# Optimization experiments

Measured on AMD Instinct MI355X. Metric: run time of the kernel, lower is better.

Reference implementation:

```python
import jax, jax.numpy as jnp
import numpy as np

N_USER = 50_000
N_ITEM = 100_000
N = N_USER + N_ITEM          # total graph nodes
E = 2_400_000                # nnz of normalized adjacency (avg degree ~16)
D = 64                       # emb_size; layers = [64, 64, 64]
SLOPE = 0.2                  # NGCF uses LeakyReLU(alpha=0.2)


def setup_inputs() -> dict:
    key = jax.random.key(0)
    ks = jax.random.split(key, 20)
    inp = {
        "user_emb": jax.random.normal(ks[0], (N_USER, D), jnp.float32) * 0.1,
        "item_emb": jax.random.normal(ks[1], (N_ITEM, D), jnp.float32) * 0.1,
    }
    for k in range(3):
        inp[f"W_gc_{k}"] = jax.random.normal(ks[2 + 4 * k], (D, D), jnp.float32) * 0.1
        inp[f"b_gc_{k}"] = jax.random.normal(ks[3 + 4 * k], (1, D), jnp.float32) * 0.1
        inp[f"W_bi_{k}"] = jax.random.normal(ks[4 + 4 * k], (D, D), jnp.float32) * 0.1
        inp[f"b_bi_{k}"] = jax.random.normal(ks[5 + 4 * k], (1, D), jnp.float32) * 0.1
    inp["adj_vals"] = jax.random.uniform(ks[14], (E,), jnp.float32) * (1.0 / 16.0)
    inp["adj_rows"] = jax.random.randint(ks[15], (E,), 0, N, jnp.int32)
    inp["adj_cols"] = jax.random.randint(ks[16], (E,), 0, N, jnp.int32)
    return inp


def _l2norm(x):
    n = jnp.linalg.norm(x, axis=1, keepdims=True)
    return x / jnp.maximum(n, 1e-12)


def reference(user_emb, item_emb,
              W_gc_0, b_gc_0, W_bi_0, b_bi_0,
              W_gc_1, b_gc_1, W_bi_1, b_bi_1,
              W_gc_2, b_gc_2, W_bi_2, b_bi_2,
              adj_vals, adj_rows, adj_cols):
    Wg = [W_gc_0, W_gc_1, W_gc_2]
    bg = [b_gc_0, b_gc_1, b_gc_2]
    Wb = [W_bi_0, W_bi_1, W_bi_2]
    bb = [b_bi_0, b_bi_1, b_bi_2]

    ego = jnp.concatenate([user_emb, item_emb], axis=0)  # [N, D]
    all_embs = [ego]
    for k in range(3):
        # side = norm_adj @ ego  (sparse COO spmm via gather + segment_sum)
        msgs = adj_vals[:, None] * ego[adj_cols]          # [E, D]
        side = jax.ops.segment_sum(msgs, adj_rows, num_segments=N)
        sum_emb = jax.nn.leaky_relu(side @ Wg[k] + bg[k], SLOPE)
        bi_emb = jax.nn.leaky_relu((ego * side) @ Wb[k] + bb[k], SLOPE)
        ego = sum_emb + bi_emb
        all_embs.append(_l2norm(ego))
    return jnp.concatenate(all_embs, axis=1)              # [N, 4*D]
```

## Files before the change

kernel.cpp:

```cpp
#include <hip/hip_runtime.h>

#define N_TOT      150000
#define N_USER     50000
#define N_EDGE     2400000
#define DIM        64
#define OUT_STRIDE 256
#define SLOPE      0.2f
#define NB_SCAN    ((N_TOT + 255) / 256)


__global__ void init_ego(const float* __restrict__ ue, const float* __restrict__ ie,
                         float* __restrict__ ego, float* __restrict__ out) {
    int idx = blockIdx.x * blockDim.x + threadIdx.x;
    if (idx >= N_TOT * DIM / 4) return;
    int n  = idx >> 4;
    int c4 = idx & 15;
    float4 v = (n < N_USER) ? ((const float4*)ue)[idx]
                            : ((const float4*)ie)[idx - N_USER * (DIM / 4)];
    ((float4*)ego)[idx] = v;
    ((float4*)out)[n * (OUT_STRIDE / 4) + c4] = v;
}

__global__ void hist_rank(const int* __restrict__ rows, int* __restrict__ cnt,
                          int* __restrict__ rank) {
    int t = blockIdx.x * blockDim.x + threadIdx.x;
    if (t >= N_EDGE / 4) return;
    int4 r4 = ((const int4*)rows)[t];
    int4 k4;
    k4.x = atomicAdd(&cnt[r4.x], 1);
    k4.y = atomicAdd(&cnt[r4.y], 1);
    k4.z = atomicAdd(&cnt[r4.z], 1);
    k4.w = atomicAdd(&cnt[r4.w], 1);
    ((int4*)rank)[t] = k4;
}

__global__ __launch_bounds__(256) void scan_partial(const int* __restrict__ cnt,
                                                    int* __restrict__ row_ptr,
                                                    int* __restrict__ bsum) {
    __shared__ int s[256];
    int tid = threadIdx.x;
    int i = blockIdx.x * 256 + tid;
    int v = (i < N_TOT) ? cnt[i] : 0;
    s[tid] = v;
    __syncthreads();
    for (int off = 1; off < 256; off <<= 1) {
        int t = (tid >= off) ? s[tid - off] : 0;
        __syncthreads();
        s[tid] += t;
        __syncthreads();
    }
    if (i < N_TOT) row_ptr[i] = s[tid] - v;
    if (tid == 255) bsum[blockIdx.x] = s[255];
}

__global__ __launch_bounds__(1024) void scan_bsums(int* __restrict__ bsum) {
    __shared__ int s[1024];
    int tid = threadIdx.x;
    int v = (tid < NB_SCAN) ? bsum[tid] : 0;
    s[tid] = v;
    __syncthreads();
    for (int off = 1; off < 1024; off <<= 1) {
        int t = (tid >= off) ? s[tid - off] : 0;
        __syncthreads();
        s[tid] += t;
        __syncthreads();
    }
    if (tid < NB_SCAN) bsum[tid] = s[tid] - v;
}

__global__ __launch_bounds__(256) void add_offsets(int* __restrict__ row_ptr,
                                                   const int* __restrict__ bsum) {
    int i = blockIdx.x * 256 + threadIdx.x;
    if (i < N_TOT) row_ptr[i] += bsum[blockIdx.x];
    if (i == 0) row_ptr[N_TOT] = N_EDGE;
}

__global__ void scatter_edges(const int* __restrict__ rows, const int* __restrict__ cols,
                              const float* __restrict__ vals,
                              const int* __restrict__ row_ptr,
                              const int* __restrict__ rank, int2* __restrict__ epack) {
    int t = blockIdx.x * blockDim.x + threadIdx.x;
    if (t >= N_EDGE / 4) return;
    int4   r4 = ((const int4*)rows)[t];
    int4   k4 = ((const int4*)rank)[t];
    int4   c4 = ((const int4*)cols)[t];
    float4 v4 = ((const float4*)vals)[t];
    epack[row_ptr[r4.x] + k4.x] = make_int2(c4.x, __float_as_int(v4.x));
    epack[row_ptr[r4.y] + k4.y] = make_int2(c4.y, __float_as_int(v4.y));
    epack[row_ptr[r4.z] + k4.z] = make_int2(c4.z, __float_as_int(v4.z));
    epack[row_ptr[r4.w] + k4.w] = make_int2(c4.w, __float_as_int(v4.w));
}

__global__ __launch_bounds__(256) void spmm_gather(
    const int* __restrict__ row_ptr, const int2* __restrict__ epack,
    const float* __restrict__ ego, float* __restrict__ side) {
    int lane = threadIdx.x & 63;
    int row  = blockIdx.x * 4 + (threadIdx.x >> 6);
    if (row >= N_TOT) return;
    int beg = row_ptr[row];
    int end = row_ptr[row + 1];
    int g = lane >> 4;
    int q = lane & 15;
    float4 acc = make_float4(0.f, 0.f, 0.f, 0.f);
    int i = beg;
    for (; i + 16 <= end; i += 16) {
        int4 e0 = ((const int4*)(epack + i))[g];
        int4 e1 = ((const int4*)(epack + i + 8))[g];
        float4 va = ((const float4*)(ego + (size_t)e0.x * DIM))[q];
        float4 vb = ((const float4*)(ego + (size_t)e0.z * DIM))[q];
        float4 vc = ((const float4*)(ego + (size_t)e1.x * DIM))[q];
        float4 vd = ((const float4*)(ego + (size_t)e1.z * DIM))[q];
        float wa = __int_as_float(e0.y);
        float wb = __int_as_float(e0.w);
        float wc = __int_as_float(e1.y);
        float wd = __int_as_float(e1.w);
        acc.x = fmaf(wa, va.x, acc.x); acc.y = fmaf(wa, va.y, acc.y);
        acc.z = fmaf(wa, va.z, acc.z); acc.w = fmaf(wa, va.w, acc.w);
        acc.x = fmaf(wb, vb.x, acc.x); acc.y = fmaf(wb, vb.y, acc.y);
        acc.z = fmaf(wb, vb.z, acc.z); acc.w = fmaf(wb, vb.w, acc.w);
        acc.x = fmaf(wc, vc.x, acc.x); acc.y = fmaf(wc, vc.y, acc.y);
        acc.z = fmaf(wc, vc.z, acc.z); acc.w = fmaf(wc, vc.w, acc.w);
        acc.x = fmaf(wd, vd.x, acc.x); acc.y = fmaf(wd, vd.y, acc.y);
        acc.z = fmaf(wd, vd.z, acc.z); acc.w = fmaf(wd, vd.w, acc.w);
    }
    for (; i + 8 <= end; i += 8) {
        int4 ee = ((const int4*)(epack + i))[g];
        float4 va = ((const float4*)(ego + (size_t)ee.x * DIM))[q];
        float4 vb = ((const float4*)(ego + (size_t)ee.z * DIM))[q];
        float wa = __int_as_float(ee.y);
        float wb = __int_as_float(ee.w);
        acc.x = fmaf(wa, va.x, acc.x); acc.y = fmaf(wa, va.y, acc.y);
        acc.z = fmaf(wa, va.z, acc.z); acc.w = fmaf(wa, va.w, acc.w);
        acc.x = fmaf(wb, vb.x, acc.x); acc.y = fmaf(wb, vb.y, acc.y);
        acc.z = fmaf(wb, vb.z, acc.z); acc.w = fmaf(wb, vb.w, acc.w);
    }
    for (; i < end; i += 4) {
        if (i + g < end) {
            int2 e = epack[i + g];
            float4 v = ((const float4*)(ego + (size_t)e.x * DIM))[q];
            float w = __int_as_float(e.y);
            acc.x = fmaf(w, v.x, acc.x); acc.y = fmaf(w, v.y, acc.y);
            acc.z = fmaf(w, v.z, acc.z); acc.w = fmaf(w, v.w, acc.w);
        }
    }
    acc.x += __shfl_xor(acc.x, 16, 64); acc.y += __shfl_xor(acc.y, 16, 64);
    acc.z += __shfl_xor(acc.z, 16, 64); acc.w += __shfl_xor(acc.w, 16, 64);
    acc.x += __shfl_xor(acc.x, 32, 64); acc.y += __shfl_xor(acc.y, 32, 64);
    acc.z += __shfl_xor(acc.z, 32, 64); acc.w += __shfl_xor(acc.w, 32, 64);
    if (g == 0)
        *(float4*)(side + (size_t)row * DIM + q * 4) = acc;
}

__global__ __launch_bounds__(256) void transform_gemm(
    const float* __restrict__ Wg, const float* __restrict__ bgv,
    const float* __restrict__ Wb, const float* __restrict__ bbv,
    const float* __restrict__ side, float* __restrict__ ego,
    float* __restrict__ out, int layer) {
    __shared__ float sST[DIM][68];
    __shared__ float sPT[DIM][68];
    __shared__ float sWg[DIM][DIM];
    __shared__ float sWb[DIM][DIM];
    int tid = threadIdx.x;
    int R0  = blockIdx.x * 64;

    #pragma unroll
    for (int it = 0; it < 4; ++it) {
        int f = tid + it * 256;
        float4 wg = ((const float4*)Wg)[f];
        float4 wb = ((const float4*)Wb)[f];
        int k = f >> 4, c = (f & 15) * 4;
        *(float4*)&sWg[k][c] = wg;
        *(float4*)&sWb[k][c] = wb;
    }
    #pragma unroll
    for (int it = 0; it < 4; ++it) {
        int f  = tid + it * 256;
        int r  = f >> 4, k0 = (f & 15) * 4;
        int row = R0 + r;
        float4 s4 = make_float4(0.f, 0.f, 0.f, 0.f);
        float4 e4 = make_float4(0.f, 0.f, 0.f, 0.f);
        if (row < N_TOT) {
            s4 = *(const float4*)&side[(size_t)row * DIM + k0];
            e4 = *(const float4*)&ego [(size_t)row * DIM + k0];
        }
        sST[k0 + 0][r] = s4.x; sST[k0 + 1][r] = s4.y;
        sST[k0 + 2][r] = s4.z; sST[k0 + 3][r] = s4.w;
        sPT[k0 + 0][r] = s4.x * e4.x; sPT[k0 + 1][r] = s4.y * e4.y;
        sPT[k0 + 2][r] = s4.z * e4.z; sPT[k0 + 3][r] = s4.w * e4.w;
    }
    __syncthreads();

    int tx = tid & 15, ty = tid >> 4;
    int c0 = tx * 4, r0 = ty * 4;
    float ag[4][4] = {{0.f}}, ab[4][4] = {{0.f}};
    #pragma unroll 4
    for (int k = 0; k < DIM; ++k) {
        float4 s4 = *(const float4*)&sST[k][r0];
        float4 p4 = *(const float4*)&sPT[k][r0];
        float4 g4 = *(const float4*)&sWg[k][c0];
        float4 b4 = *(const float4*)&sWb[k][c0];
        float ss[4] = {s4.x, s4.y, s4.z, s4.w};
        float pp[4] = {p4.x, p4.y, p4.z, p4.w};
        float gg[4] = {g4.x, g4.y, g4.z, g4.w};
        float bw[4] = {b4.x, b4.y, b4.z, b4.w};
        #pragma unroll
        for (int i = 0; i < 4; ++i)
            #pragma unroll
            for (int j = 0; j < 4; ++j) {
                ag[i][j] = fmaf(ss[i], gg[j], ag[i][j]);
                ab[i][j] = fmaf(pp[i], bw[j], ab[i][j]);
            }
    }

    float4 bg4 = *(const float4*)&bgv[c0];
    float4 bb4 = *(const float4*)&bbv[c0];
    float bgl[4] = {bg4.x, bg4.y, bg4.z, bg4.w};
    float bbl[4] = {bb4.x, bb4.y, bb4.z, bb4.w};

    float ne[4][4];
    float ss2[4];
    #pragma unroll
    for (int i = 0; i < 4; ++i) {
        float s = 0.f;
        #pragma unroll
        for (int j = 0; j < 4; ++j) {
            float g = ag[i][j] + bgl[j];
            float b = ab[i][j] + bbl[j];
            g = g > 0.f ? g : SLOPE * g;
            b = b > 0.f ? b : SLOPE * b;
            float v = g + b;
            ne[i][j] = v;
            s = fmaf(v, v, s);
        }
        ss2[i] = s;
    }
    #pragma unroll
    for (int m = 1; m < 16; m <<= 1) {
        #pragma unroll
        for (int i = 0; i < 4; ++i) ss2[i] += __shfl_xor(ss2[i], m, 64);
    }

    float* outbase = out + (size_t)(layer + 1) * DIM;
    #pragma unroll
    for (int i = 0; i < 4; ++i) {
        int row = R0 + r0 + i;
        if (row >= N_TOT) break;
        float inv = 1.f / fmaxf(sqrtf(ss2[i]), 1e-12f);
        float4 e4 = make_float4(ne[i][0], ne[i][1], ne[i][2], ne[i][3]);
        float4 o4 = make_float4(ne[i][0] * inv, ne[i][1] * inv, ne[i][2] * inv, ne[i][3] * inv);
        *(float4*)&ego[(size_t)row * DIM + c0] = e4;
        *(float4*)&outbase[(size_t)row * OUT_STRIDE + c0] = o4;
    }
}

extern "C" void kernel_launch(void* const* d_in, const int* in_sizes, int n_in,
                              void* d_out, int out_size, void* d_ws, size_t ws_size,
                              hipStream_t stream) {
    const float* ue = (const float*)d_in[0];
    const float* ie = (const float*)d_in[1];
    const float* Wg[3] = {(const float*)d_in[2], (const float*)d_in[6], (const float*)d_in[10]};
    const float* bg[3] = {(const float*)d_in[3], (const float*)d_in[7], (const float*)d_in[11]};
    const float* Wb[3] = {(const float*)d_in[4], (const float*)d_in[8], (const float*)d_in[12]};
    const float* bb[3] = {(const float*)d_in[5], (const float*)d_in[9], (const float*)d_in[13]};
    const float* vals = (const float*)d_in[14];
    const int*  rows  = (const int*)d_in[15];
    const int*  cols  = (const int*)d_in[16];
    float* out = (float*)d_out;

    float* ego     = (float*)d_ws;
    float* side    = ego + (size_t)N_TOT * DIM;
    int2*  epack   = (int2*)(side + (size_t)N_TOT * DIM);
    int*   row_ptr = (int*)(epack + N_EDGE);
    int*   cnt     = row_ptr + (N_TOT + 16);
    int*   bsum    = cnt + N_TOT;
    int*   rank    = (int*)side;

    hipMemsetAsync(cnt, 0, (size_t)N_TOT * sizeof(int), stream);
    hist_rank<<<(N_EDGE / 4 + 255) / 256, 256, 0, stream>>>(rows, cnt, rank);
    scan_partial<<<NB_SCAN, 256, 0, stream>>>(cnt, row_ptr, bsum);
    scan_bsums<<<1, 1024, 0, stream>>>(bsum);
    add_offsets<<<NB_SCAN, 256, 0, stream>>>(row_ptr, bsum);
    scatter_edges<<<(N_EDGE / 4 + 255) / 256, 256, 0, stream>>>(rows, cols, vals,
                                                                row_ptr, rank, epack);

    init_ego<<<(N_TOT * DIM / 4 + 255) / 256, 256, 0, stream>>>(ue, ie, ego, out);

    for (int k = 0; k < 3; ++k) {
        spmm_gather<<<(N_TOT + 3) / 4, 256, 0, stream>>>(row_ptr, epack, ego, side);
        transform_gemm<<<(N_TOT + 63) / 64, 256, 0, stream>>>(Wg[k], bg[k], Wb[k], bb[k],
                                                              side, ego, out, k);
    }
}
```

Measured before the change: 794.7 us.

## Unroll SpMM gather to 32 edges and load GEMM activations directly into registers

The SpMM gather loop now handles 32 edges per iteration with eight independent row loads in flight, to expose more memory-level parallelism for the random gathers. The transform GEMM no longer stages side and ego tiles transposed through shared memory. Each thread reads its own four rows straight from global memory in float4 chunks, which cuts shared memory use and its bank-conflicting transposed writes. The cost is that each side/ego row is loaded 16 times across the threads covering its columns, relying on cache, and register pressure rises in both kernels. Average degree is about 16, so many rows never reach the 32-edge loop and fall through to the shorter tails.

```diff
diff --git a/kernel.cpp b/kernel.cpp
--- a/kernel.cpp
+++ b/kernel.cpp
@@ -103,17 +103,23 @@
     int q = lane & 15;
     float4 acc = make_float4(0.f, 0.f, 0.f, 0.f);
     int i = beg;
-    for (; i + 16 <= end; i += 16) {
+    for (; i + 32 <= end; i += 32) {
         int4 e0 = ((const int4*)(epack + i))[g];
         int4 e1 = ((const int4*)(epack + i + 8))[g];
+        int4 e2 = ((const int4*)(epack + i + 16))[g];
+        int4 e3 = ((const int4*)(epack + i + 24))[g];
         float4 va = ((const float4*)(ego + (size_t)e0.x * DIM))[q];
         float4 vb = ((const float4*)(ego + (size_t)e0.z * DIM))[q];
         float4 vc = ((const float4*)(ego + (size_t)e1.x * DIM))[q];
         float4 vd = ((const float4*)(ego + (size_t)e1.z * DIM))[q];
-        float wa = __int_as_float(e0.y);
-        float wb = __int_as_float(e0.w);
-        float wc = __int_as_float(e1.y);
-        float wd = __int_as_float(e1.w);
+        float4 ve = ((const float4*)(ego + (size_t)e2.x * DIM))[q];
+        float4 vf = ((const float4*)(ego + (size_t)e2.z * DIM))[q];
+        float4 vg = ((const float4*)(ego + (size_t)e3.x * DIM))[q];
+        float4 vh = ((const float4*)(ego + (size_t)e3.z * DIM))[q];
+        float wa = __int_as_float(e0.y), wb = __int_as_float(e0.w);
+        float wc = __int_as_float(e1.y), wd = __int_as_float(e1.w);
+        float we = __int_as_float(e2.y), wf = __int_as_float(e2.w);
+        float wg = __int_as_float(e3.y), wh = __int_as_float(e3.w);
         acc.x = fmaf(wa, va.x, acc.x); acc.y = fmaf(wa, va.y, acc.y);
         acc.z = fmaf(wa, va.z, acc.z); acc.w = fmaf(wa, va.w, acc.w);
         acc.x = fmaf(wb, vb.x, acc.x); acc.y = fmaf(wb, vb.y, acc.y);
@@ -122,6 +128,14 @@
         acc.z = fmaf(wc, vc.z, acc.z); acc.w = fmaf(wc, vc.w, acc.w);
         acc.x = fmaf(wd, vd.x, acc.x); acc.y = fmaf(wd, vd.y, acc.y);
         acc.z = fmaf(wd, vd.z, acc.z); acc.w = fmaf(wd, vd.w, acc.w);
+        acc.x = fmaf(we, ve.x, acc.x); acc.y = fmaf(we, ve.y, acc.y);
+        acc.z = fmaf(we, ve.z, acc.z); acc.w = fmaf(we, ve.w, acc.w);
+        acc.x = fmaf(wf, vf.x, acc.x); acc.y = fmaf(wf, vf.y, acc.y);
+        acc.z = fmaf(wf, vf.z, acc.z); acc.w = fmaf(wf, vf.w, acc.w);
+        acc.x = fmaf(wg, vg.x, acc.x); acc.y = fmaf(wg, vg.y, acc.y);
+        acc.z = fmaf(wg, vg.z, acc.z); acc.w = fmaf(wg, vg.w, acc.w);
+        acc.x = fmaf(wh, vh.x, acc.x); acc.y = fmaf(wh, vh.y, acc.y);
+        acc.z = fmaf(wh, vh.z, acc.z); acc.w = fmaf(wh, vh.w, acc.w);
     }
     for (; i + 8 <= end; i += 8) {
         int4 ee = ((const int4*)(epack + i))[g];
@@ -156,8 +170,6 @@
     const float* __restrict__ Wb, const float* __restrict__ bbv,
     const float* __restrict__ side, float* __restrict__ ego,
     float* __restrict__ out, int layer) {
-    __shared__ float sST[DIM][68];
-    __shared__ float sPT[DIM][68];
     __shared__ float sWg[DIM][DIM];
     __shared__ float sWb[DIM][DIM];
     int tid = threadIdx.x;
@@ -172,44 +184,45 @@
         *(float4*)&sWg[k][c] = wg;
         *(float4*)&sWb[k][c] = wb;
     }
-    #pragma unroll
-    for (int it = 0; it < 4; ++it) {
-        int f  = tid + it * 256;
-        int r  = f >> 4, k0 = (f & 15) * 4;
-        int row = R0 + r;
-        float4 s4 = make_float4(0.f, 0.f, 0.f, 0.f);
-        float4 e4 = make_float4(0.f, 0.f, 0.f, 0.f);
-        if (row < N_TOT) {
-            s4 = *(const float4*)&side[(size_t)row * DIM + k0];
-            e4 = *(const float4*)&ego [(size_t)row * DIM + k0];
-        }
-        sST[k0 + 0][r] = s4.x; sST[k0 + 1][r] = s4.y;
-        sST[k0 + 2][r] = s4.z; sST[k0 + 3][r] = s4.w;
-        sPT[k0 + 0][r] = s4.x * e4.x; sPT[k0 + 1][r] = s4.y * e4.y;
-        sPT[k0 + 2][r] = s4.z * e4.z; sPT[k0 + 3][r] = s4.w * e4.w;
-    }
     __syncthreads();
 
     int tx = tid & 15, ty = tid >> 4;
     int c0 = tx * 4, r0 = ty * 4;
+    int rowbase = R0 + r0;
     float ag[4][4] = {{0.f}}, ab[4][4] = {{0.f}};
-    #pragma unroll 4
-    for (int k = 0; k < DIM; ++k) {
-        float4 s4 = *(const float4*)&sST[k][r0];
-        float4 p4 = *(const float4*)&sPT[k][r0];
-        float4 g4 = *(const float4*)&sWg[k][c0];
-        float4 b4 = *(const float4*)&sWb[k][c0];
-        float ss[4] = {s4.x, s4.y, s4.z, s4.w};
-        float pp[4] = {p4.x, p4.y, p4.z, p4.w};
-        float gg[4] = {g4.x, g4.y, g4.z, g4.w};
-        float bw[4] = {b4.x, b4.y, b4.z, b4.w};
+
+    for (int k0 = 0; k0 < DIM; k0 += 4) {
+        float sreg[4][4], preg[4][4];
         #pragma unroll
-        for (int i = 0; i < 4; ++i)
+        for (int i = 0; i < 4; ++i) {
+            int row = rowbase + i;
+            float4 sv = make_float4(0.f, 0.f, 0.f, 0.f);
+            float4 ev = make_float4(0.f, 0.f, 0.f, 0.f);
+            if (row < N_TOT) {
+                sv = *(const float4*)&side[(size_t)row * DIM + k0];
+                ev = *(const float4*)&ego [(size_t)row * DIM + k0];
+            }
+            sreg[i][0] = sv.x; sreg[i][1] = sv.y; sreg[i][2] = sv.z; sreg[i][3] = sv.w;
+            preg[i][0] = sv.x * ev.x; preg[i][1] = sv.y * ev.y;
+            preg[i][2] = sv.z * ev.z; preg[i][3] = sv.w * ev.w;
+        }
+        #pragma unroll
+        for (int kk = 0; kk < 4; ++kk) {
+            float4 g4 = *(const float4*)&sWg[k0 + kk][c0];
+            float4 b4 = *(const float4*)&sWb[k0 + kk][c0];
+            float gg[4] = {g4.x, g4.y, g4.z, g4.w};
+            float bw[4] = {b4.x, b4.y, b4.z, b4.w};
             #pragma unroll
-            for (int j = 0; j < 4; ++j) {
-                ag[i][j] = fmaf(ss[i], gg[j], ag[i][j]);
-                ab[i][j] = fmaf(pp[i], bw[j], ab[i][j]);
+            for (int i = 0; i < 4; ++i) {
+                float ss = sreg[i][kk];
+                float pp = preg[i][kk];
+                #pragma unroll
+                for (int j = 0; j < 4; ++j) {
+                    ag[i][j] = fmaf(ss, gg[j], ag[i][j]);
+                    ab[i][j] = fmaf(pp, bw[j], ab[i][j]);
+                }
             }
+        }
     }
 
     float4 bg4 = *(const float4*)&bgv[c0];
@@ -243,7 +256,7 @@
     float* outbase = out + (size_t)(layer + 1) * DIM;
     #pragma unroll
     for (int i = 0; i < 4; ++i) {
-        int row = R0 + r0 + i;
+        int row = rowbase + i;
         if (row >= N_TOT) break;
         float inv = 1.f / fmaxf(sqrtf(ss2[i]), 1e-12f);
         float4 e4 = make_float4(ne[i][0], ne[i][1], ne[i][2], ne[i][3]);
```

After: 863.5 us. 8.7% more time.
